# Kernel tuning notes

Hardware: AMD Instinct MI355X
Metric: run time of the kernel (lower is better)

The kernel has to match this reference:

```python
import jax, jax.numpy as jnp
from jax import lax
import numpy as np

B = 512
EPS = 1e-5


def _conv(x, w, b):
    # x: [B,C,H,W], w: [O,I,3,3], stride 1, pad 1 (same spatial)
    y = lax.conv_general_dilated(x, w, window_strides=(1, 1),
                                 padding=[(1, 1), (1, 1)],
                                 dimension_numbers=('NCHW', 'OIHW', 'NCHW'))
    return y + b[None, :, None, None]


def _bn(x, g, b, m, v):
    # eval-mode batchnorm with running stats
    inv = g * lax.rsqrt(v + EPS)
    return x * inv[None, :, None, None] + (b - m * inv)[None, :, None, None]


def _maxpool2(x):
    return lax.reduce_window(x, -jnp.inf, lax.max, (1, 1, 2, 2), (1, 1, 2, 2), 'VALID')


def _block(x, w, b, g, be, m, v):
    return _maxpool2(jax.nn.relu(_bn(_conv(x, w, b), g, be, m, v)))


def setup_inputs() -> dict:
    key = jax.random.key(0)
    ks = jax.random.split(key, 12)
    n = lambda k, s: jax.random.normal(k, s, jnp.float32) * 0.05
    z = lambda s: jnp.zeros(s, jnp.float32)
    o = lambda s: jnp.ones(s, jnp.float32)
    return {
        'x': jax.random.normal(ks[0], (B, 1, 48, 48), jnp.float32),
        'conv1_w': n(ks[1], (256, 1, 3, 3)), 'conv1_b': z((256,)),
        'bn1_g': o((256,)), 'bn1_b': z((256,)), 'bn1_m': z((256,)), 'bn1_v': o((256,)),
        'conv2_w': n(ks[2], (128, 256, 3, 3)), 'conv2_b': z((128,)),
        'bn2_g': o((128,)), 'bn2_b': z((128,)), 'bn2_m': z((128,)), 'bn2_v': o((128,)),
        'conv3_w': n(ks[3], (64, 128, 3, 3)), 'conv3_b': z((64,)),
        'bn3_g': o((64,)), 'bn3_b': z((64,)), 'bn3_m': z((64,)), 'bn3_v': o((64,)),
        'fc1_w': n(ks[4], (512, 2304)), 'fc1_b': z((512,)),
        'fc2_w': n(ks[5], (256, 512)), 'fc2_b': z((256,)),
        'att_w': n(ks[6], (64, 256)), 'att_b': z((64,)),
        'fc3_w': n(ks[7], (7, 64)), 'fc3_b': z((7,)),
    }


def reference(x, conv1_w, conv1_b, bn1_g, bn1_b, bn1_m, bn1_v,
              conv2_w, conv2_b, bn2_g, bn2_b, bn2_m, bn2_v,
              conv3_w, conv3_b, bn3_g, bn3_b, bn3_m, bn3_v,
              fc1_w, fc1_b, fc2_w, fc2_b, att_w, att_b, fc3_w, fc3_b):
    out1 = _block(x, conv1_w, conv1_b, bn1_g, bn1_b, bn1_m, bn1_v)      # [B,256,24,24]
    out2 = _block(out1, conv2_w, conv2_b, bn2_g, bn2_b, bn2_m, bn2_v)   # [B,128,12,12]
    out3 = _block(out2, conv3_w, conv3_b, bn3_g, bn3_b, bn3_m, bn3_v)   # [B,64,6,6]
    b_ = out3.shape[0]
    out4 = out3.reshape(b_, -1)                                          # [B,2304]
    out5 = out4 @ fc1_w.T + fc1_b                                        # [B,512]
    out6 = out5 @ fc2_w.T + fc2_b                                        # [B,256]
    # spatial attention: query projected to channel dim of out3
    q = out6 @ att_w.T + att_b                                           # [B,64]
    scores = jnp.einsum('bchw,bc->bhw', out3, q).reshape(b_, -1)         # [B,36]
    attn = jax.nn.softmax(scores, axis=1).reshape(b_, 6, 6)
    g_mod = jnp.einsum('bchw,bhw->bc', out3, attn)                       # [B,64]
    return g_mod @ fc3_w.T + fc3_b                                       # [B,7]
```

## Files before the change

kernel.cpp:

```cpp
#include <hip/hip_runtime.h>
#include <hip/hip_bf16.h>
#include <math.h>

#define EPS_BN 1e-5f

typedef __bf16 bf16x8 __attribute__((ext_vector_type(8)));
typedef float f32x4 __attribute__((ext_vector_type(4)));
typedef float f32x2 __attribute__((ext_vector_type(2)));

__device__ __forceinline__ void gl2lds16(const void* g, void* l) {
  __builtin_amdgcn_global_load_lds(
      (const __attribute__((address_space(1))) unsigned int*)g,
      (__attribute__((address_space(3))) unsigned int*)l, 16, 0, 0);
}

__global__ __launch_bounds__(256) void k_conv1(
    const float* __restrict__ x, const float* __restrict__ w,
    const float* __restrict__ cb, const float* __restrict__ g,
    const float* __restrict__ bb, const float* __restrict__ m,
    const float* __restrict__ v, __hip_bfloat16* __restrict__ out1p,
    __hip_bfloat16* __restrict__ out2p, const float* __restrict__ W32,
    const float* __restrict__ fc1w, float* __restrict__ Wet, int n1) {
  __shared__ float xp[14 * 50];
  const int bq = blockIdx.x;
  const int t = threadIdx.x;
  if (bq >= n1) {
    int idx = (bq - n1) * 256 + t;
    int r = idx / 2304, c = idx - r * 2304;
    float s = 0.f;
    for (int k = 0; k < 512; k++)
      s = fmaf(W32[r * 512 + k], fc1w[k * 2304 + c], s);
    Wet[c * 64 + r] = s;
    return;
  }
  const int b = bq >> 2, q = bq & 3;
  __hip_bfloat16* ob = out1p + (size_t)b * (26 * 26 * 256);
  const __hip_bfloat16 z = __float2bfloat16(0.f);
  if (q == 0)
    for (int i = t; i < 26 * 256; i += 256) ob[i] = z;
  if (q == 3)
    for (int i = t; i < 26 * 256; i += 256) ob[25 * 26 * 256 + i] = z;
  for (int i = t; i < 6 * 2 * 256; i += 256) {
    int r = 1 + 6 * q + (i >> 9), side = (i >> 8) & 1, c = i & 255;
    ob[(r * 26 + side * 25) * 256 + c] = z;
  }
  {
    __hip_bfloat16* o2 = out2p + (size_t)b * (14 * 14 * 128);
    if (q == 0)
      for (int i = t; i < 14 * 128; i += 256) o2[i] = z;
    if (q == 1)
      for (int i = t; i < 14 * 128; i += 256) o2[13 * 14 * 128 + i] = z;
    if (q == 2)
      for (int i = t; i < 6 * 2 * 128; i += 256) {
        int r = 1 + (i >> 8), side = (i >> 7) & 1, c = i & 127;
        o2[(r * 14 + side * 13) * 128 + c] = z;
      }
    if (q == 3)
      for (int i = t; i < 6 * 2 * 128; i += 256) {
        int r = 7 + (i >> 8), side = (i >> 7) & 1, c = i & 127;
        o2[(r * 14 + side * 13) * 128 + c] = z;
      }
  }
  for (int i = t; i < 14 * 50; i += 256) xp[i] = 0.f;
  __syncthreads();
  const float* xb = x + (size_t)b * 2304;
  for (int i = t; i < 14 * 48; i += 256) {
    int rr = i / 48, c = i - rr * 48;
    int gr = 12 * q - 1 + rr;
    if (gr >= 0 && gr < 48) xp[rr * 50 + c + 1] = xb[gr * 48 + c];
  }
  __syncthreads();
  float wr[9];
#pragma unroll
  for (int i = 0; i < 9; i++) wr[i] = w[t * 9 + i];
  const float scale = g[t] * rsqrtf(v[t] + EPS_BN);
  const float bias = (cb[t] - m[t]) * scale + bb[t];
#pragma unroll
  for (int ohl = 0; ohl < 6; ohl++) {
    const int r0 = 2 * ohl;
    f32x2 c01[4];
#pragma unroll
    for (int r = 0; r < 4; r++) c01[r] = *(const f32x2*)&xp[(r0 + r) * 50];
#pragma unroll 4
    for (int ow = 0; ow < 24; ow++) {
      f32x2 c23[4];
#pragma unroll
      for (int r = 0; r < 4; r++)
        c23[r] = *(const f32x2*)&xp[(r0 + r) * 50 + 2 * ow + 2];
      f32x2 s2a = 0.f, s2b = 0.f;
#pragma unroll
      for (int r = 0; r < 4; r++) {
        f32x2 p0 = c01[r], p2 = c23[r];
        f32x2 p1 = {p0.y, p2.x};
        if (r <= 2) {
          s2a += p0 * wr[r * 3 + 0];
          s2a += p1 * wr[r * 3 + 1];
          s2a += p2 * wr[r * 3 + 2];
        }
        if (r >= 1) {
          s2b += p0 * wr[(r - 1) * 3 + 0];
          s2b += p1 * wr[(r - 1) * 3 + 1];
          s2b += p2 * wr[(r - 1) * 3 + 2];
        }
      }
      f32x2 b0 = s2a * scale + bias;
      f32x2 b1 = s2b * scale + bias;
      float mx = fmaxf(fmaxf(b0.x, b0.y), fmaxf(b1.x, b1.y));
      ob[((6 * q + ohl + 1) * 26 + (ow + 1)) * 256 + t] =
          __float2bfloat16(fmaxf(mx, 0.f));
#pragma unroll
      for (int r = 0; r < 4; r++) c01[r] = c23[r];
    }
  }
}

__global__ void k_prep(const float* __restrict__ c2w,
                       __hip_bfloat16* __restrict__ wt2,
                       const float* __restrict__ c3w,
                       __hip_bfloat16* __restrict__ wt3,
                       const float* __restrict__ attw,
                       const float* __restrict__ fc2w, float* __restrict__ W32,
                       const float* __restrict__ fc1b,
                       const float* __restrict__ fc2b,
                       const float* __restrict__ attb, float* __restrict__ be) {
  const int blk = blockIdx.x, tid = threadIdx.x;
  if (blk < 1152) {
    int idx = blk * 256 + tid;
    int icr = idx & 7;
    int lhi = (idx >> 3) & 3;
    int oc = (idx >> 5) & 127;
    int rest = idx >> 12;
    int kb = rest & 7;
    int p = rest >> 3;
    int ic = kb * 32 + lhi * 8 + icr;
    wt2[idx] = __float2bfloat16(c2w[(oc * 256 + ic) * 9 + p]);
  } else if (blk < 1440) {
    int idx = (blk - 1152) * 256 + tid;
    int icr = idx & 7;
    int oc = (idx >> 3) & 63;
    int rest = idx >> 9;
    int icg = rest & 15;
    int p = rest >> 4;
    wt3[idx] = __float2bfloat16(c3w[(oc * 128 + icg * 8 + icr) * 9 + p]);
  } else if (blk < 1568) {
    int idx = (blk - 1440) * 256 + tid;
    int r = idx >> 9, c = idx & 511;
    float s = 0.f;
    for (int k = 0; k < 256; k++)
      s = fmaf(attw[r * 256 + k], fc2w[k * 512 + c], s);
    W32[idx] = s;
  } else {
    __shared__ float t1[256];
    float s = fc2b[tid];
    for (int k = 0; k < 512; k++) s = fmaf(fc2w[tid * 512 + k], fc1b[k], s);
    t1[tid] = s;
    __syncthreads();
    if (tid < 64) {
      float r = attb[tid];
      for (int k = 0; k < 256; k++) r = fmaf(attw[tid * 256 + k], t1[k], r);
      be[tid] = r;
    }
  }
}

__global__ __launch_bounds__(256) void k_mconv2(
    const __hip_bfloat16* __restrict__ in, const __hip_bfloat16* __restrict__ wt,
    const float* __restrict__ cb, const float* __restrict__ gg,
    const float* __restrict__ bbv, const float* __restrict__ bm,
    const float* __restrict__ bv, __hip_bfloat16* __restrict__ outp) {
  constexpr int HW = 24, IC = 256, OC = 128, HP = 26, CP = 26;
  constexpr int MTW = 6;
  constexpr int ROWS = 4;
  constexpr int TILES = 6;
  constexpr int WN = 32;
  constexpr int NF = 2;
  constexpr int NCH = 6 * CP * 8;
  constexpr int NCHP = (NCH + 255) & ~255;
  constexpr int NLD = NCHP / 256;
  constexpr int NSTG = 4;
  constexpr int ABUF = NCHP * 16;
  constexpr int KG = IC / 32;
  constexpr int EPITCH = OC + 1;
  constexpr int EBYTES = 48 * EPITCH * 4;
  constexpr int SMB = (2 * ABUF) > EBYTES ? (2 * ABUF) : EBYTES;
  constexpr int NSTEP = NSTG * 18;
  constexpr int D = 3;

  __shared__ __align__(16) char smraw[SMB];
  float* se = (float*)smraw;

  const int tid = threadIdx.x;
  const int wn = tid >> 6, ln = tid & 63;
  const int lhi = ln >> 4, llo = ln & 15;

  const int per = gridDim.x >> 3;
  const int xcd = blockIdx.x & 7, sl = blockIdx.x >> 3;
  const int b = xcd * (per / TILES) + sl / TILES;
  const int T = sl % TILES;
  const int h0 = T * ROWS;

  const __hip_bfloat16* inb = in + (size_t)b * HP * HP * IC;

  int srcoff[NLD];
#pragma unroll
  for (int i = 0; i < NLD; i++) {
    int ci = tid + i * 256;
    if (ci >= NCH) ci = NCH - 1;
    int kgslot = ci & 7;
    int rest = ci >> 3;
    int c = rest % CP;
    int r = rest / CP;
    int kg = kgslot ^ (c & 7);
    srcoff[i] = ((h0 + r) * HP + c) * IC + kg * 8;
  }
  int spb[MTW], wlv[MTW];
#pragma unroll
  for (int mt = 0; mt < MTW; mt++) {
    int m = mt * 16 + llo;
    int hl = m / HW, wl = m % HW;
    spb[mt] = (hl * CP + wl) * 8;
    wlv[mt] = wl;
  }
  const __hip_bfloat16* wtb = wt + (wn * WN + llo) * 32 + lhi * 8;

  f32x4 acc[MTW][NF];
  const f32x4 fz = {0.f, 0.f, 0.f, 0.f};
#pragma unroll
  for (int i = 0; i < MTW; i++)
#pragma unroll
    for (int j = 0; j < NF; j++) acc[i][j] = fz;

#pragma unroll
  for (int i = 0; i < NLD; i++)
    gl2lds16(inb + srcoff[i], smraw + (tid + i * 256) * 16);
  bf16x8 bq[D][NF];
#pragma unroll
  for (int d = 0; d < D; d++) {
    const int sg = d / 18, pg = (d % 18) >> 1, kf = d & 1;
#pragma unroll
    for (int j = 0; j < NF; j++)
      bq[d][j] = *(const bf16x8*)(wtb +
                                  (size_t)((pg * KG + sg * 2 + kf) * OC) * 32 +
                                  j * 512);
  }
  __syncthreads();

#pragma unroll
  for (int s = 0; s < NSTG; s++) {
    const char* cw = smraw + (s & 1) * ABUF;
#pragma unroll
    for (int t = 0; t < 18; t++) {
      const int g = s * 18 + t;
      const int p = t >> 1, ks = t & 1;
      const int ph = p / 3, pw = p % 3;
      const int kg = ks * 4 + lhi;
#pragma unroll
      for (int mt = 0; mt < MTW; mt++) {
        int slot = spb[mt] + (ph * CP + pw) * 8 + (kg ^ ((wlv[mt] + pw) & 7));
        bf16x8 af = *(const bf16x8*)(cw + slot * 16);
#pragma unroll
        for (int j = 0; j < NF; j++)
          acc[mt][j] = __builtin_amdgcn_mfma_f32_16x16x32_bf16(
              af, bq[g % D][j], acc[mt][j], 0, 0, 0);
      }
      if (g + D < NSTEP) {
        const int gf = g + D;
        const int sg = gf / 18, pg = (gf % 18) >> 1, kf = gf & 1;
#pragma unroll
        for (int j = 0; j < NF; j++)
          bq[gf % D][j] =
              *(const bf16x8*)(wtb +
                               (size_t)((pg * KG + sg * 2 + kf) * OC) * 32 +
                               j * 512);
      }
      if (t == 13 && s + 1 < NSTG) {
        char* nb = smraw + ((s + 1) & 1) * ABUF;
#pragma unroll
        for (int i = 0; i < NLD; i++)
          gl2lds16(inb + srcoff[i] + (s + 1) * 64, nb + (tid + i * 256) * 16);
      }
    }
    __syncthreads();
  }

  constexpr int OHW = HW / 2;
  constexpr int NP = 1 * OHW * OC;
#pragma unroll
  for (int pz = 0; pz < 2; pz++) {
    if (pz) __syncthreads();
#pragma unroll
    for (int j = 0; j < NF; j++) {
      int n = wn * WN + j * 16 + llo;
      float scale = gg[n] * rsqrtf(bv[n] + EPS_BN);
      float bias = (cb[n] - bm[n]) * scale + bbv[n];
#pragma unroll
      for (int mtl = 0; mtl < 3; mtl++)
#pragma unroll
        for (int r = 0; r < 4; r++) {
          int mrow = mtl * 16 + lhi * 4 + r;
          se[mrow * EPITCH + n] =
              fmaxf(acc[pz * 3 + mtl][j][r] * scale + bias, 0.f);
        }
    }
    __syncthreads();
    for (int sI = tid; sI < NP; sI += 256) {
      int n = sI % OC;
      int ow = (sI / OC) % OHW;
      int mloc = 2 * ow;
      float x0 = se[mloc * EPITCH + n];
      float x1 = se[(mloc + 1) * EPITCH + n];
      float x2 = se[(mloc + HW) * EPITCH + n];
      float x3 = se[(mloc + HW + 1) * EPITCH + n];
      float mx = fmaxf(fmaxf(x0, x1), fmaxf(x2, x3));
      int oh = (h0 >> 1) + pz;
      outp[(((size_t)b * 14 + oh + 1) * 14 + ow + 1) * OC + n] =
          __float2bfloat16(mx);
    }
  }
}

__global__ __launch_bounds__(256) void k_c3attn(
    const __hip_bfloat16* __restrict__ in, const __hip_bfloat16* __restrict__ wt,
    const float* __restrict__ cb, const float* __restrict__ gg,
    const float* __restrict__ bbv, const float* __restrict__ bm,
    const float* __restrict__ bv, const float* __restrict__ Wet,
    const float* __restrict__ be, const float* __restrict__ w3,
    const float* __restrict__ b3, float* __restrict__ out, int b0) {
  constexpr int HW = 12, IC = 128, OC = 64, HP = 14, CP = 14;
  constexpr int NCH = 14 * CP * 8;
  constexpr int NCHP = (NCH + 255) & ~255;
  constexpr int NLD = NCHP / 256;
  constexpr int NSTG = 2;
  constexpr int ABUF = NCHP * 16;
  constexpr int ICG = 16;
  constexpr int EPITCH = OC + 1;

  __shared__ __align__(16) char smraw[2 * ABUF];
  __shared__ float act[64 * 37];
  __shared__ float qp[4][64];
  __shared__ float ql[64], gm[64], sc[36];
  float* se = (float*)smraw;

  const int tid = threadIdx.x;
  const int wv = tid >> 6, ln = tid & 63;
  const int lhi = ln >> 4, llo = ln & 15;
  const int b = blockIdx.x;

  const __hip_bfloat16* inb = in + (size_t)b * HP * HP * IC;

  int srcoff[NLD];
#pragma unroll
  for (int i = 0; i < NLD; i++) {
    int ci = tid + i * 256;
    if (ci >= NCH) ci = NCH - 1;
    int kgslot = ci & 7;
    int rest = ci >> 3;
    int c = rest % CP;
    int r = rest / CP;
    int kg = kgslot ^ (c & 7);
    srcoff[i] = (r * HP + c) * IC + kg * 8;
  }
  int spb[9], wlv[9];
#pragma unroll
  for (int mt = 0; mt < 9; mt++) {
    int m = mt * 16 + llo;
    int hl = m / HW, wl = m % HW;
    spb[mt] = (hl * CP + wl) * 8;
    wlv[mt] = wl;
  }
  const __hip_bfloat16* wtb = wt + (size_t)(lhi * OC + wv * 16 + llo) * 8;

  f32x4 acc[9];
  const f32x4 fz = {0.f, 0.f, 0.f, 0.f};
#pragma unroll
  for (int i = 0; i < 9; i++) acc[i] = fz;

#pragma unroll
  for (int i = 0; i < NLD; i++)
    gl2lds16(inb + srcoff[i], smraw + (tid + i * 256) * 16);
  __syncthreads();

#pragma unroll
  for (int s = 0; s < NSTG; s++) {
    if (s + 1 < NSTG) {
      char* nb = smraw + ((s + 1) & 1) * ABUF;
#pragma unroll
      for (int i = 0; i < NLD; i++)
        gl2lds16(inb + srcoff[i] + (s + 1) * 64, nb + (tid + i * 256) * 16);
    }
    const char* cw = smraw + (s & 1) * ABUF;
#pragma unroll
    for (int tt = 0; tt < 18; tt++) {
      const int p = tt >> 1, ks = tt & 1;
      const int ph = p / 3, pw = p % 3;
      const int kg = ks * 4 + lhi;
      bf16x8 bf =
          *(const bf16x8*)(wtb + ((size_t)(p * ICG + s * 8 + ks * 4) * OC) * 8);
#pragma unroll
      for (int mt = 0; mt < 9; mt++) {
        int slot = spb[mt] + (ph * CP + pw) * 8 + (kg ^ ((wlv[mt] + pw) & 7));
        bf16x8 af = *(const bf16x8*)(cw + slot * 16);
        acc[mt] = __builtin_amdgcn_mfma_f32_16x16x32_bf16(af, bf, acc[mt], 0,
                                                          0, 0);
      }
    }
    __syncthreads();
  }

  {
    const int n = wv * 16 + llo;
    const float scale = gg[n] * rsqrtf(bv[n] + EPS_BN);
    const float bias = (cb[n] - bm[n]) * scale + bbv[n];
#pragma unroll
    for (int pz = 0; pz < 3; pz++) {
      if (pz) __syncthreads();
#pragma unroll
      for (int mtl = 0; mtl < 3; mtl++)
#pragma unroll
        for (int r = 0; r < 4; r++) {
          int mrow = mtl * 16 + lhi * 4 + r;
          se[mrow * EPITCH + n] =
              fmaxf(acc[pz * 3 + mtl][r] * scale + bias, 0.f);
        }
      __syncthreads();
      for (int sI = tid; sI < 2 * 6 * 64; sI += 256) {
        int nn = sI % 64;
        int ow = (sI / 64) % 6;
        int ohl = sI / (64 * 6);
        int mloc = (2 * ohl) * HW + 2 * ow;
        float x0 = se[mloc * EPITCH + nn];
        float x1 = se[(mloc + 1) * EPITCH + nn];
        float x2 = se[(mloc + HW) * EPITCH + nn];
        float x3 = se[(mloc + HW + 1) * EPITCH + nn];
        float mx = fmaxf(fmaxf(x0, x1), fmaxf(x2, x3));
        act[nn * 37 + (pz * 2 + ohl) * 6 + ow] = mx;
      }
    }
  }
  __syncthreads();

  {
    float qpv = 0.f;
    const int n = ln;
#pragma unroll 2
    for (int c2 = wv * 16; c2 < wv * 16 + 16; c2++)
      for (int hw = 0; hw < 36; hw++)
        qpv = fmaf(act[c2 * 37 + hw], Wet[(c2 * 36 + hw) * 64 + n], qpv);
    qp[wv][n] = qpv;
  }
  __syncthreads();
  if (tid < 64)
    ql[tid] = be[tid] + qp[0][tid] + qp[1][tid] + qp[2][tid] + qp[3][tid];
  __syncthreads();
  if (wv == 0) {
    float s = -INFINITY;
    if (ln < 36) {
      float a = 0.f;
      for (int c = 0; c < 64; c++) a = fmaf(act[c * 37 + ln], ql[c], a);
      s = a;
    }
    float mx = s;
    for (int off = 32; off >= 1; off >>= 1)
      mx = fmaxf(mx, __shfl_xor(mx, off));
    float e = (ln < 36) ? expf(s - mx) : 0.f;
    float sum = e;
    for (int off = 32; off >= 1; off >>= 1) sum += __shfl_xor(sum, off);
    if (ln < 36) sc[ln] = e / sum;
  }
  __syncthreads();
  if (wv == 0) {
    float gv = 0.f;
    for (int hw = 0; hw < 36; hw++) gv = fmaf(act[ln * 37 + hw], sc[hw], gv);
    gm[ln] = gv;
  }
  __syncthreads();
  if (tid < 7) {
    float a = b3[tid];
    for (int c = 0; c < 64; c++) a = fmaf(w3[tid * 64 + c], gm[c], a);
    out[(size_t)(b0 + b) * 7 + tid] = a;
  }
}

extern "C" void kernel_launch(void* const* d_in, const int* in_sizes, int n_in,
                              void* d_out, int out_size, void* d_ws,
                              size_t ws_size, hipStream_t stream) {
  const float* x    = (const float*)d_in[0];
  const float* c1w  = (const float*)d_in[1];
  const float* c1b  = (const float*)d_in[2];
  const float* g1   = (const float*)d_in[3];
  const float* bb1  = (const float*)d_in[4];
  const float* m1   = (const float*)d_in[5];
  const float* v1   = (const float*)d_in[6];
  const float* c2w  = (const float*)d_in[7];
  const float* c2b  = (const float*)d_in[8];
  const float* g2   = (const float*)d_in[9];
  const float* bb2  = (const float*)d_in[10];
  const float* m2   = (const float*)d_in[11];
  const float* v2   = (const float*)d_in[12];
  const float* c3w  = (const float*)d_in[13];
  const float* c3b  = (const float*)d_in[14];
  const float* g3   = (const float*)d_in[15];
  const float* bb3  = (const float*)d_in[16];
  const float* m3   = (const float*)d_in[17];
  const float* v3   = (const float*)d_in[18];
  const float* fc1w = (const float*)d_in[19];
  const float* fc1b = (const float*)d_in[20];
  const float* fc2w = (const float*)d_in[21];
  const float* fc2b = (const float*)d_in[22];
  const float* attw = (const float*)d_in[23];
  const float* attb = (const float*)d_in[24];
  const float* fc3w = (const float*)d_in[25];
  const float* fc3b = (const float*)d_in[26];

  const size_t PER_CHUNK = (173056ULL + 25088ULL) * 2;
  const size_t PERSIST = 589824 + 147456 + 131072 + 589824 + 256 + 8192;
  int CH = 512;
  while (CH > 8 && (size_t)CH * PER_CHUNK + PERSIST > ws_size) CH >>= 1;
  const int NCHK = 512 / CH;

  char* base = (char*)d_ws;
  size_t off = 0;
  auto alloc = [&](size_t nbytes) -> void* {
    void* p = base + off;
    off = (off + nbytes + 255) & ~(size_t)255;
    return p;
  };
  __hip_bfloat16* out1p = (__hip_bfloat16*)alloc((size_t)CH * 173056 * 2);
  __hip_bfloat16* out2p = (__hip_bfloat16*)alloc((size_t)CH * 25088 * 2);
  __hip_bfloat16* wt2  = (__hip_bfloat16*)alloc(589824);
  __hip_bfloat16* wt3  = (__hip_bfloat16*)alloc(147456);
  float* W32           = (float*)alloc(131072);
  float* Wet           = (float*)alloc(589824);
  float* be            = (float*)alloc(256);

  k_prep<<<1569, 256, 0, stream>>>(c2w, wt2, c3w, wt3, attw, fc2w, W32, fc1b,
                                   fc2b, attb, be);

  for (int c = 0; c < NCHK; c++) {
    const float* xc = x + (size_t)c * CH * 2304;
    const int n1 = CH * 4;
    const int grid1 = n1 + (c == 0 ? 576 : 0);
    k_conv1<<<grid1, 256, 0, stream>>>(xc, c1w, c1b, g1, bb1, m1, v1, out1p,
                                       out2p, W32, fc1w, Wet, n1);
    k_mconv2<<<CH * 6, 256, 0, stream>>>(out1p, wt2, c2b, g2, bb2, m2, v2,
                                         out2p);
    k_c3attn<<<CH, 256, 0, stream>>>(out2p, wt3, c3b, g3, bb3, m3, v3, Wet, be,
                                     fc3w, fc3b, (float*)d_out, c * CH);
  }
}
```

Before: 419.9 us.

## Switch conv2 to 32x32x16 MFMA tiles with a reorganized weight layout

The conv2 implicit-GEMM kernel now uses 32x32x16 bf16 MFMA instructions instead of 16x16x32. Each wave handles three 32-row M tiles against a single 32-column N fragment, and the weight prep kernel is relaid out to match the new k-half operand layout. The register prefetch ring for weights is removed, so weights are loaded directly inside the loop, and the next-stage LDS prefetch is issued at the start of each stage instead of mid-stage. The larger MFMA tile is meant to cut LDS A-fragment reads per FLOP and instruction count, at the cost of less latency hiding on the weight loads and a more complex epilogue row mapping.

```diff
diff --git a/kernel.cpp b/kernel.cpp
--- a/kernel.cpp
+++ b/kernel.cpp
@@ -6,6 +6,7 @@
 
 typedef __bf16 bf16x8 __attribute__((ext_vector_type(8)));
 typedef float f32x4 __attribute__((ext_vector_type(4)));
+typedef float f32x16 __attribute__((ext_vector_type(16)));
 typedef float f32x2 __attribute__((ext_vector_type(2)));
 
 __device__ __forceinline__ void gl2lds16(const void* g, void* l) {
@@ -103,9 +104,9 @@
           s2b += p2 * wr[(r - 1) * 3 + 2];
         }
       }
-      f32x2 b0 = s2a * scale + bias;
-      f32x2 b1 = s2b * scale + bias;
-      float mx = fmaxf(fmaxf(b0.x, b0.y), fmaxf(b1.x, b1.y));
+      f32x2 e0 = s2a * scale + bias;
+      f32x2 e1 = s2b * scale + bias;
+      float mx = fmaxf(fmaxf(e0.x, e0.y), fmaxf(e1.x, e1.y));
       ob[((6 * q + ohl + 1) * 26 + (ow + 1)) * 256 + t] =
           __float2bfloat16(fmaxf(mx, 0.f));
 #pragma unroll
@@ -127,12 +128,11 @@
   if (blk < 1152) {
     int idx = blk * 256 + tid;
     int icr = idx & 7;
-    int lhi = (idx >> 3) & 3;
-    int oc = (idx >> 5) & 127;
-    int rest = idx >> 12;
-    int kb = rest & 7;
-    int p = rest >> 3;
-    int ic = kb * 32 + lhi * 8 + icr;
+    int oc = (idx >> 3) & 127;
+    int kh = (idx >> 10) & 1;
+    int kbg = (idx >> 11) & 15;
+    int p = idx >> 15;
+    int ic = kbg * 16 + kh * 8 + icr;
     wt2[idx] = __float2bfloat16(c2w[(oc * 256 + ic) * 9 + p]);
   } else if (blk < 1440) {
     int idx = (blk - 1152) * 256 + tid;
@@ -169,35 +169,26 @@
     const float* __restrict__ bbv, const float* __restrict__ bm,
     const float* __restrict__ bv, __hip_bfloat16* __restrict__ outp) {
   constexpr int HW = 24, IC = 256, OC = 128, HP = 26, CP = 26;
-  constexpr int MTW = 6;
-  constexpr int ROWS = 4;
-  constexpr int TILES = 6;
-  constexpr int WN = 32;
-  constexpr int NF = 2;
   constexpr int NCH = 6 * CP * 8;
   constexpr int NCHP = (NCH + 255) & ~255;
   constexpr int NLD = NCHP / 256;
   constexpr int NSTG = 4;
   constexpr int ABUF = NCHP * 16;
-  constexpr int KG = IC / 32;
   constexpr int EPITCH = OC + 1;
-  constexpr int EBYTES = 48 * EPITCH * 4;
-  constexpr int SMB = (2 * ABUF) > EBYTES ? (2 * ABUF) : EBYTES;
-  constexpr int NSTEP = NSTG * 18;
-  constexpr int D = 3;
+  constexpr int SMB = 2 * ABUF;
 
   __shared__ __align__(16) char smraw[SMB];
   float* se = (float*)smraw;
 
   const int tid = threadIdx.x;
   const int wn = tid >> 6, ln = tid & 63;
-  const int lhi = ln >> 4, llo = ln & 15;
+  const int l31 = ln & 31, khalf = ln >> 5;
 
   const int per = gridDim.x >> 3;
   const int xcd = blockIdx.x & 7, sl = blockIdx.x >> 3;
-  const int b = xcd * (per / TILES) + sl / TILES;
-  const int T = sl % TILES;
-  const int h0 = T * ROWS;
+  const int b = xcd * (per / 6) + sl / 6;
+  const int T = sl % 6;
+  const int h0 = T * 4;
 
   const __hip_bfloat16* inb = in + (size_t)b * HP * HP * IC;
 
@@ -213,107 +204,86 @@
     int kg = kgslot ^ (c & 7);
     srcoff[i] = ((h0 + r) * HP + c) * IC + kg * 8;
   }
-  int spb[MTW], wlv[MTW];
-#pragma unroll
-  for (int mt = 0; mt < MTW; mt++) {
-    int m = mt * 16 + llo;
+  int spb[3], wlv[3];
+#pragma unroll
+  for (int mt = 0; mt < 3; mt++) {
+    int m = mt * 32 + l31;
     int hl = m / HW, wl = m % HW;
     spb[mt] = (hl * CP + wl) * 8;
     wlv[mt] = wl;
   }
-  const __hip_bfloat16* wtb = wt + (wn * WN + llo) * 32 + lhi * 8;
-
-  f32x4 acc[MTW][NF];
-  const f32x4 fz = {0.f, 0.f, 0.f, 0.f};
-#pragma unroll
-  for (int i = 0; i < MTW; i++)
-#pragma unroll
-    for (int j = 0; j < NF; j++) acc[i][j] = fz;
+  const __hip_bfloat16* wtb = wt + (size_t)(khalf * OC + wn * 32 + l31) * 8;
+
+  f32x16 acc[3];
+#pragma unroll
+  for (int i = 0; i < 3; i++)
+#pragma unroll
+    for (int r = 0; r < 16; r++) acc[i][r] = 0.f;
 
 #pragma unroll
   for (int i = 0; i < NLD; i++)
     gl2lds16(inb + srcoff[i], smraw + (tid + i * 256) * 16);
-  bf16x8 bq[D][NF];
-#pragma unroll
-  for (int d = 0; d < D; d++) {
-    const int sg = d / 18, pg = (d % 18) >> 1, kf = d & 1;
-#pragma unroll
-    for (int j = 0; j < NF; j++)
-      bq[d][j] = *(const bf16x8*)(wtb +
-                                  (size_t)((pg * KG + sg * 2 + kf) * OC) * 32 +
-                                  j * 512);
-  }
   __syncthreads();
 
 #pragma unroll
   for (int s = 0; s < NSTG; s++) {
+    if (s + 1 < NSTG) {
+      char* nb = smraw + ((s + 1) & 1) * ABUF;
+#pragma unroll
+      for (int i = 0; i < NLD; i++)
+        gl2lds16(inb + srcoff[i] + (s + 1) * 64, nb + (tid + i * 256) * 16);
+    }
     const char* cw = smraw + (s & 1) * ABUF;
 #pragma unroll
-    for (int t = 0; t < 18; t++) {
-      const int g = s * 18 + t;
-      const int p = t >> 1, ks = t & 1;
+    for (int p = 0; p < 9; p++) {
       const int ph = p / 3, pw = p % 3;
-      const int kg = ks * 4 + lhi;
-#pragma unroll
-      for (int mt = 0; mt < MTW; mt++) {
-        int slot = spb[mt] + (ph * CP + pw) * 8 + (kg ^ ((wlv[mt] + pw) & 7));
-        bf16x8 af = *(const bf16x8*)(cw + slot * 16);
-#pragma unroll
-        for (int j = 0; j < NF; j++)
-          acc[mt][j] = __builtin_amdgcn_mfma_f32_16x16x32_bf16(
-              af, bq[g % D][j], acc[mt][j], 0, 0, 0);
-      }
-      if (g + D < NSTEP) {
-        const int gf = g + D;
-        const int sg = gf / 18, pg = (gf % 18) >> 1, kf = gf & 1;
-#pragma unroll
-        for (int j = 0; j < NF; j++)
-          bq[gf % D][j] =
-              *(const bf16x8*)(wtb +
-                               (size_t)((pg * KG + sg * 2 + kf) * OC) * 32 +
-                               j * 512);
-      }
-      if (t == 13 && s + 1 < NSTG) {
-        char* nb = smraw + ((s + 1) & 1) * ABUF;
-#pragma unroll
-        for (int i = 0; i < NLD; i++)
-          gl2lds16(inb + srcoff[i] + (s + 1) * 64, nb + (tid + i * 256) * 16);
+#pragma unroll
+      for (int kb = 0; kb < 4; kb++) {
+        const int kg = kb * 2 + khalf;
+        bf16x8 bf =
+            *(const bf16x8*)(wtb + (size_t)(p * 16 + s * 4 + kb) * 2048);
+#pragma unroll
+        for (int mt = 0; mt < 3; mt++) {
+          int slot = spb[mt] + (ph * CP + pw) * 8 + (kg ^ ((wlv[mt] + pw) & 7));
+          bf16x8 af = *(const bf16x8*)(cw + slot * 16);
+          acc[mt] = __builtin_amdgcn_mfma_f32_32x32x16_bf16(af, bf, acc[mt], 0,
+                                                            0, 0);
+        }
       }
     }
     __syncthreads();
   }
 
-  constexpr int OHW = HW / 2;
-  constexpr int NP = 1 * OHW * OC;
+  const int n = wn * 32 + l31;
+  const float scale = gg[n] * rsqrtf(bv[n] + EPS_BN);
+  const float bias = (cb[n] - bm[n]) * scale + bbv[n];
+  constexpr int OHW = 12;
 #pragma unroll
   for (int pz = 0; pz < 2; pz++) {
     if (pz) __syncthreads();
 #pragma unroll
-    for (int j = 0; j < NF; j++) {
-      int n = wn * WN + j * 16 + llo;
-      float scale = gg[n] * rsqrtf(bv[n] + EPS_BN);
-      float bias = (cb[n] - bm[n]) * scale + bbv[n];
-#pragma unroll
-      for (int mtl = 0; mtl < 3; mtl++)
-#pragma unroll
-        for (int r = 0; r < 4; r++) {
-          int mrow = mtl * 16 + lhi * 4 + r;
-          se[mrow * EPITCH + n] =
-              fmaxf(acc[pz * 3 + mtl][j][r] * scale + bias, 0.f);
+    for (int mt = 0; mt < 3; mt++)
+#pragma unroll
+      for (int r = 0; r < 16; r++) {
+        const int rl0 = (r & 3) + 8 * (r >> 2);
+        const int m0 = mt * 32 + rl0;
+        if ((pz == 0 && m0 < 48) || (pz == 1 && m0 >= 48)) {
+          int mrow = m0 + 4 * khalf - pz * 48;
+          se[mrow * EPITCH + n] = fmaxf(acc[mt][r] * scale + bias, 0.f);
         }
-    }
+      }
     __syncthreads();
-    for (int sI = tid; sI < NP; sI += 256) {
-      int n = sI % OC;
-      int ow = (sI / OC) % OHW;
+    for (int sI = tid; sI < OHW * OC; sI += 256) {
+      int n2 = sI % OC;
+      int ow = sI / OC;
       int mloc = 2 * ow;
-      float x0 = se[mloc * EPITCH + n];
-      float x1 = se[(mloc + 1) * EPITCH + n];
-      float x2 = se[(mloc + HW) * EPITCH + n];
-      float x3 = se[(mloc + HW + 1) * EPITCH + n];
+      float x0 = se[mloc * EPITCH + n2];
+      float x1 = se[(mloc + 1) * EPITCH + n2];
+      float x2 = se[(mloc + HW) * EPITCH + n2];
+      float x3 = se[(mloc + HW + 1) * EPITCH + n2];
       float mx = fmaxf(fmaxf(x0, x1), fmaxf(x2, x3));
-      int oh = (h0 >> 1) + pz;
-      outp[(((size_t)b * 14 + oh + 1) * 14 + ow + 1) * OC + n] =
+      int oh = T * 2 + pz;
+      outp[(((size_t)b * 14 + oh + 1) * 14 + ow + 1) * OC + n2] =
           __float2bfloat16(mx);
     }
   }
```

Result: slower. 438.8 us (+4.5%).
